# Kernel tuning notes

Hardware: AMD Instinct MI355X
Metric: run time of the kernel (lower is better)

Reference implementation:

```python
import jax, jax.numpy as jnp
import numpy as np

EPS = 1e-5
BS, NA, NC, NL, NPTS, ED, NG = 1, 900, 6, 4, 13, 256, 8
GD = ED // NG
IMG_W, IMG_H = 704.0, 256.0
FMAP_HW = [(64, 176), (32, 88), (16, 44), (8, 22)]


def _ln(x, g, b):
    m = x.mean(-1, keepdims=True)
    v = ((x - m) ** 2).mean(-1, keepdims=True)
    return (x - m) / jnp.sqrt(v + EPS) * g + b


def _grid_sample(img, grid):
    # img: [N,C,H,W]; grid: [N,P,Q,2] in [-1,1]; bilinear, zeros padding, align_corners=False
    N, C, H, W = img.shape
    gx = jnp.clip((grid[..., 0] + 1.0) * (W * 0.5) - 0.5, -1e4, 1e4)
    gy = jnp.clip((grid[..., 1] + 1.0) * (H * 0.5) - 0.5, -1e4, 1e4)
    x0 = jnp.floor(gx); y0 = jnp.floor(gy)
    wx1 = gx - x0; wy1 = gy - y0; wx0 = 1.0 - wx1; wy0 = 1.0 - wy1
    x0i = x0.astype(jnp.int32); y0i = y0.astype(jnp.int32)
    flat = img.reshape(N, C, H * W)

    def corner(xi, yi, wgt):
        valid = (xi >= 0) & (xi < W) & (yi >= 0) & (yi < H)
        idx = (jnp.clip(yi, 0, H - 1) * W + jnp.clip(xi, 0, W - 1))
        g = jax.vmap(lambda f, i: f[:, i])(flat, idx.reshape(N, -1))  # [N,C,P*Q]
        g = g.reshape(N, C, idx.shape[1], idx.shape[2])
        return g * (wgt * valid)[:, None]

    return (corner(x0i, y0i, wx0 * wy0) + corner(x0i + 1, y0i, wx1 * wy0)
            + corner(x0i, y0i + 1, wx0 * wy1) + corner(x0i + 1, y0i + 1, wx1 * wy1))


def setup_inputs() -> dict:
    key = jax.random.key(0)
    ks = jax.random.split(key, 20)
    d = {}
    d['instance_feature'] = jax.random.normal(ks[0], (BS, NA, ED), jnp.float32)
    xyz = jax.random.normal(ks[1], (BS, NA, 3), jnp.float32) * 1.5
    size = jax.random.normal(ks[2], (BS, NA, 3), jnp.float32) * 0.3
    theta = jax.random.uniform(ks[3], (BS, NA, 1), jnp.float32) * (2.0 * np.pi)
    vel = jax.random.normal(ks[4], (BS, NA, 3), jnp.float32) * 0.1
    d['anchor'] = jnp.concatenate([xyz, size, jnp.sin(theta), jnp.cos(theta), vel], -1)
    d['anchor_embed'] = jax.random.normal(ks[5], (BS, NA, ED), jnp.float32)
    for i, (h, w) in enumerate(FMAP_HW):
        d[f'fmap{i}'] = jax.random.normal(ks[6 + i], (BS, NC, ED, h, w), jnp.float32)
    base = jnp.array([[80., 0., 0., 352.], [0., 80., 0., 128.],
                      [0., 0., 0., 1.], [0., 0., 0., 1.]], jnp.float32)
    proj = jnp.tile(base, (BS, NC, 1, 1))
    proj = proj.at[:, :, :2, :].add(jax.random.normal(ks[10], (BS, NC, 2, 4), jnp.float32) * 2.0)
    d['projection_mat'] = proj
    d['image_wh'] = jnp.broadcast_to(jnp.array([IMG_W, IMG_H], jnp.float32), (BS, NC, 2))
    d['fix_scale'] = jnp.array([[0, 0, 0], [0.45, 0, 0], [-0.45, 0, 0], [0, 0.45, 0],
                                [0, -0.45, 0], [0, 0, 0.45], [0, 0, -0.45]], jnp.float32)

    def w(k, shape):
        return jax.random.normal(k, shape, jnp.float32) * 0.02

    d['lfc_w'] = w(ks[11], (ED, 6 * 3)); d['lfc_b'] = jnp.zeros((18,), jnp.float32)
    d['cam_w1'] = w(ks[12], (12, ED)); d['cam_b1'] = jnp.zeros((ED,), jnp.float32)
    d['cam_g1'] = jnp.ones((ED,), jnp.float32); d['cam_be1'] = jnp.zeros((ED,), jnp.float32)
    d['cam_w2'] = w(ks[13], (ED, ED)); d['cam_b2'] = jnp.zeros((ED,), jnp.float32)
    d['cam_g2'] = jnp.ones((ED,), jnp.float32); d['cam_be2'] = jnp.zeros((ED,), jnp.float32)
    d['wfc_w'] = w(ks[14], (ED, NG * NL * NPTS)); d['wfc_b'] = jnp.zeros((NG * NL * NPTS,), jnp.float32)
    d['op_w'] = w(ks[15], (ED, ED)); d['op_b'] = jnp.zeros((ED,), jnp.float32)
    return d


def reference(instance_feature, anchor, anchor_embed, fmap0, fmap1, fmap2, fmap3,
              projection_mat, image_wh, fix_scale, lfc_w, lfc_b,
              cam_w1, cam_b1, cam_g1, cam_be1, cam_w2, cam_b2, cam_g2, cam_be2,
              wfc_w, wfc_b, op_w, op_b):
    bs, na = instance_feature.shape[:2]
    # ---- keypoint generation ----
    size = jnp.exp(anchor[..., None, 3:6])                       # [bs,na,1,3]
    kp = fix_scale * size                                        # [bs,na,7,3]
    ls = jax.nn.sigmoid(instance_feature @ lfc_w + lfc_b).reshape(bs, na, -1, 3) - 0.5
    kp = jnp.concatenate([kp, ls * size], axis=-2)               # [bs,na,NPTS,3]
    sin, cos = anchor[..., 6:7], anchor[..., 7:8]                # [bs,na,1]
    kx, ky, kz = kp[..., 0], kp[..., 1], kp[..., 2]
    key_points = jnp.stack([cos * kx - sin * ky, sin * kx + cos * ky, kz], -1) \
                 + anchor[..., None, 0:3]                        # [bs,na,NPTS,3]
    # ---- per-cam/level/point group weights ----
    feat = instance_feature + anchor_embed
    cam_in = projection_mat[:, :, :3].reshape(bs, NC, 12)
    h = jax.nn.relu(cam_in @ cam_w1 + cam_b1); h = _ln(h, cam_g1, cam_be1)
    h = jax.nn.relu(h @ cam_w2 + cam_b2); cam_embed = _ln(h, cam_g2, cam_be2)
    f = feat[:, :, None] + cam_embed[:, None]                    # [bs,na,NC,ED]
    wts = (f @ wfc_w + wfc_b).reshape(bs, na, NC * NL * NPTS, NG)
    wts = jax.nn.softmax(wts, axis=-2).reshape(bs, na, NC, NL, NPTS, NG)
    # ---- multi-cam projection + bilinear sampling ----
    pts = jnp.concatenate([key_points, jnp.ones_like(key_points[..., :1])], -1)
    p2d = jnp.einsum('bcij,banj->bcani', projection_mat, pts)    # [bs,NC,na,NPTS,4]
    p2d = p2d[..., :2] / jnp.maximum(p2d[..., 2:3], 1e-5)
    p2d = p2d / image_wh[:, :, None, None]
    grid = (p2d * 2.0 - 1.0).reshape(bs * NC, na, NPTS, 2)
    feats = jnp.stack([_grid_sample(fm.reshape(bs * NC, ED, fm.shape[-2], fm.shape[-1]), grid)
                       for fm in (fmap0, fmap1, fmap2, fmap3)], axis=1)  # [bs*NC,NL,ED,na,NPTS]
    feats = feats.reshape(bs, NC, NL, ED, na, NPTS).transpose(0, 4, 1, 2, 5, 3)  # [bs,na,NC,NL,NPTS,ED]
    # ---- group-weighted fusion over cams & levels, then sum over points ----
    fg = feats.reshape(bs, na, NC, NL, NPTS, NG, GD)
    fused = jnp.einsum('bnclpg,bnclpgd->bnpgd', wts, fg).reshape(bs, na, NPTS, ED)
    fused = fused.sum(axis=2)                                    # [bs,na,ED]
    out = fused @ op_w + op_b
    return jnp.concatenate([out, instance_feature], axis=-1)     # [bs,na,2*ED]
```

## Files before the change

### kernel.cpp

```cpp
#include <hip/hip_runtime.h>
#include <stdint.h>

#define NA 900
#define NC 6
#define NL 4
#define NPTS 13
#define ED 256
#define NG 8
#define LNEPS 1e-5f
#define NSTAGE 718303
#define NSTAGE_BLOCKS 2806
#define NTRANS 5616
#define NSAMP 312

struct PIn { const void* p[24]; };

__device__ __forceinline__ float b2f(unsigned short u){
  union { uint32_t i; float f; } v; v.i = ((uint32_t)u)<<16; return v.f;
}
__device__ __forceinline__ unsigned short f2b(float f){
  union { float f; uint32_t i; } v; v.f = f;
  uint32_t r = v.i + 0x7FFFu + ((v.i>>16)&1u);
  return (unsigned short)(r>>16);
}
#define BLO(u) __uint_as_float((u)<<16)
#define BHI(u) __uint_as_float((u)&0xffff0000u)

__device__ __forceinline__ float ldx(const void* p, int i, bool bf){
  return bf ? b2f(((const unsigned short*)p)[i]) : ((const float*)p)[i];
}

__device__ __forceinline__ bool sniff_bf(const unsigned short* __restrict__ u16){
  int lane = threadIdx.x & 63;
  unsigned short u = u16[2*lane];
  int e = (u>>7)&0xFF;
  int sane = (e>=110 && e<=135) ? 1 : 0;
  #pragma unroll
  for (int m=32;m;m>>=1) sane += __shfl_xor(sane, m);
  return sane >= 48;
}

__device__ __forceinline__ void blockReduce2(float& a, float& b, float* lds){
  #pragma unroll
  for (int m=32;m;m>>=1){ a += __shfl_xor(a,m); b += __shfl_xor(b,m); }
  int w = threadIdx.x>>6;
  if ((threadIdx.x&63)==0){ lds[w]=a; lds[w+4]=b; }
  __syncthreads();
  a = lds[0]+lds[1]+lds[2]+lds[3];
  b = lds[4]+lds[5]+lds[6]+lds[7];
  __syncthreads();
}

__global__ __launch_bounds__(256) void k_prep(PIn in, float* __restrict__ stage,
                                              unsigned short* __restrict__ tf,
                                              float* __restrict__ Bc){
  const bool bf = sniff_bf((const unsigned short*)in.p[0]);
  const int tid = threadIdx.x;
  int b = blockIdx.x;

  __shared__ unsigned short T[64][68];
  __shared__ float h[ED];
  __shared__ float cE[ED];
  __shared__ float red8[8];
  __shared__ float part[4][64];

  if (b < NSTAGE_BLOCKS){
    const int cum[21] = {0,230400,240300,470700,470796,470808,470829,475437,475455,
                         478527,478783,479039,479295,544831,545087,545343,545599,
                         652095,652511,718047,718303};
    const int map[20] = {0,1,2,7,8,9,10,11,12,13,14,15,16,17,18,19,20,21,22,23};
    int idx = b*256 + tid;
    if (idx >= NSTAGE) return;
    int seg = 0, base = 0;
    #pragma unroll
    for (int s=1;s<20;s++) if (idx >= cum[s]){ seg = s; base = cum[s]; }
    const void* src = in.p[map[0]];
    #pragma unroll
    for (int s=1;s<20;s++) if (seg==s) src = in.p[map[s]];
    stage[idx] = ldx(src, idx - base, bf);
    return;
  }
  b -= NSTAGE_BLOCKS;
  if (b < NTRANS){
    const int xb[4]  = {176,44,11,3};
    const int HWs[4] = {11264,2816,704,176};
    const int TFO[4] = {0,17301504,21626880,22708224};
    int l, local;
    if      (b < 4224){ l=0; local=b;      }
    else if (b < 5280){ l=1; local=b-4224; }
    else if (b < 5544){ l=2; local=b-5280; }
    else              { l=3; local=b-5544; }
    int pt = local % xb[l]; int rest = local / xb[l];
    int ct = rest & 3; int c = rest >> 2;
    const int HW = HWs[l];
    const int px0 = pt*64;
    const void* src = in.p[3+l];
    #pragma unroll
    for (int p=0;p<2;p++){
      int lch = p*32 + (tid>>3);
      int gch = ct*64 + lch;
      int pxv = (tid&7)*8;
      size_t base = (size_t)(c*ED+gch)*HW + px0 + pxv;
      unsigned short v[8];
      if (px0 + pxv + 8 <= HW){
        if (bf){
          uint4 q = *reinterpret_cast<const uint4*>((const unsigned short*)src + base);
          v[0]=q.x&0xffff; v[1]=q.x>>16; v[2]=q.y&0xffff; v[3]=q.y>>16;
          v[4]=q.z&0xffff; v[5]=q.z>>16; v[6]=q.w&0xffff; v[7]=q.w>>16;
        } else {
          float4 f0 = *reinterpret_cast<const float4*>((const float*)src + base);
          float4 f1 = *reinterpret_cast<const float4*>((const float*)src + base + 4);
          v[0]=f2b(f0.x); v[1]=f2b(f0.y); v[2]=f2b(f0.z); v[3]=f2b(f0.w);
          v[4]=f2b(f1.x); v[5]=f2b(f1.y); v[6]=f2b(f1.z); v[7]=f2b(f1.w);
        }
      } else {
        #pragma unroll
        for (int i=0;i<8;i++){
          int px = px0+pxv+i;
          v[i] = (px<HW) ? (bf ? ((const unsigned short*)src)[base+i]
                               : f2b(((const float*)src)[base+i])) : (unsigned short)0;
        }
      }
      #pragma unroll
      for (int i=0;i<8;i++) T[pxv+i][lch] = v[i];
    }
    __syncthreads();
    unsigned short* dst = tf + TFO[l] + (size_t)c*HW*ED + ct*64;
    #pragma unroll
    for (int p=0;p<2;p++){
      int pxl = p*32 + (tid>>3);
      int px = px0 + pxl;
      if (px >= HW) continue;
      int ch8 = (tid&7)*8;
      ushort4 lo = *reinterpret_cast<ushort4*>(&T[pxl][ch8]);
      ushort4 hi = *reinterpret_cast<ushort4*>(&T[pxl][ch8+4]);
      union { ushort4 hh[2]; uint4 q; } u;
      u.hh[0]=lo; u.hh[1]=hi;
      *reinterpret_cast<uint4*>(dst + (size_t)px*ED + ch8) = u.q;
    }
    return;
  }
  b -= NTRANS;
  {
    const void* proj = in.p[7];
    const void* w1 = in.p[12]; const void* b1 = in.p[13];
    const void* g1 = in.p[14]; const void* be1 = in.p[15];
    const void* w2 = in.p[16]; const void* b2 = in.p[17];
    const void* g2 = in.p[18]; const void* be2 = in.p[19];
    const void* wfcw = in.p[20]; const void* wfcb = in.p[21];
    const int c = b/7, colt = b - (b/7)*7;
    float ci[12];
    #pragma unroll
    for (int i=0;i<12;i++) ci[i] = ldx(proj, c*16+i, bf);
    float acc = ldx(b1, tid, bf);
    #pragma unroll
    for (int k=0;k<12;k++) acc += ci[k]*ldx(w1, k*ED+tid, bf);
    float x = fmaxf(acc, 0.f);
    float s=x, q=x*x;
    blockReduce2(s,q,red8);
    float mean = s*(1.f/ED), var = q*(1.f/ED)-mean*mean;
    h[tid] = (x-mean)*rsqrtf(var+LNEPS)*ldx(g1,tid,bf) + ldx(be1,tid,bf);
    __syncthreads();
    acc = ldx(b2, tid, bf);
    #pragma unroll 8
    for (int k=0;k<ED;k++) acc += h[k]*ldx(w2, k*ED+tid, bf);
    x = fmaxf(acc,0.f);
    s=x; q=x*x;
    blockReduce2(s,q,red8);
    mean = s*(1.f/ED); var = q*(1.f/ED)-mean*mean;
    cE[tid] = (x-mean)*rsqrtf(var+LNEPS)*ldx(g2,tid,bf) + ldx(be2,tid,bf);
    __syncthreads();
    const int kc = tid>>6, colL = tid&63, col = colt*64+colL;
    float a = 0.f;
    if (col < 416){
      #pragma unroll 8
      for (int k=0;k<64;k++) a += cE[kc*64+k]*ldx(wfcw, (kc*64+k)*416+col, bf);
    }
    part[kc][colL] = a;
    __syncthreads();
    if (kc==0 && col<416)
      Bc[c*416+col] = part[0][colL]+part[1][colL]+part[2][colL]+part[3][colL] + ldx(wfcb,col,bf);
  }
}

__global__ __launch_bounds__(256) void k_anchor(
    const float* __restrict__ stage, const unsigned short* __restrict__ tf,
    const float* __restrict__ Bc, const void* __restrict__ rawinst,
    void* __restrict__ outv){
  const int n = blockIdx.x, tid = threadIdx.x;
  const bool bf = sniff_bf((const unsigned short*)rawinst);

  const float* s_inst = stage + 0;
  const float* s_anc  = stage + 230400;
  const float* s_ae   = stage + 240300;
  const float* s_proj = stage + 470700;
  const float* s_imwh = stage + 470796;
  const float* s_fixs = stage + 470808;
  const float* s_lw   = stage + 470829;
  const float* s_lb   = stage + 475437;
  const float* s_wfcw = stage + 545599;
  const float* s_opw  = stage + 652511;
  const float* s_opb  = stage + 718047;

  __shared__ float ifs[ED];
  __shared__ float fe[ED];
  __shared__ float lg[NC*416];
  __shared__ uint4 dsc[NSAMP*2];
  __shared__ float red[8][ED];
  __shared__ float fu[ED];
  __shared__ float kp[13][3];
  __shared__ float sc[8];
  __shared__ float lsv[18];

  {
    float iv = s_inst[n*ED+tid];
    ifs[tid] = iv;
    fe[tid]  = iv + s_ae[n*ED+tid];
    if (tid < 3)       sc[tid] = s_anc[n*11+tid];
    else if (tid == 3) sc[3]   = s_anc[n*11+6];
    else if (tid == 4) sc[4]   = s_anc[n*11+7];
    else if (tid < 8)  sc[tid] = __expf(s_anc[n*11+tid-2]);
  }
  __syncthreads();
  if (tid < 144){
    int d = tid>>3, j = tid&7;
    float a = 0.f;
    #pragma unroll 8
    for (int k=j*32;k<j*32+32;k++) a += ifs[k]*s_lw[k*18+d];
    a += __shfl_xor(a,1); a += __shfl_xor(a,2); a += __shfl_xor(a,4);
    if (j==0){
      a += s_lb[d];
      lsv[d] = 1.f/(1.f+__expf(-a)) - 0.5f;
    }
  }
  __syncthreads();
  if (tid < 13){
    float kx,ky,kz;
    if (tid < 7){
      kx = s_fixs[tid*3+0]*sc[5];
      ky = s_fixs[tid*3+1]*sc[6];
      kz = s_fixs[tid*3+2]*sc[7];
    } else {
      int j = tid-7;
      kx = lsv[j*3+0]*sc[5]; ky = lsv[j*3+1]*sc[6]; kz = lsv[j*3+2]*sc[7];
    }
    kp[tid][0] = sc[4]*kx - sc[3]*ky + sc[0];
    kp[tid][1] = sc[3]*kx + sc[4]*ky + sc[1];
    kp[tid][2] = kz + sc[2];
  }
  {
    int col2 = (tid < 160) ? tid+256 : 415;
    float a0 = 0.f, a1 = 0.f;
    #pragma unroll 4
    for (int k=0;k<ED;k++){
      float fv = fe[k];
      a0 += fv*s_wfcw[k*416+tid];
      a1 += fv*s_wfcw[k*416+col2];
    }
    #pragma unroll
    for (int c=0;c<NC;c++){
      lg[c*416+tid] = a0 + Bc[c*416+tid];
      if (tid < 160) lg[c*416+tid+256] = a1 + Bc[c*416+tid+256];
    }
  }
  __syncthreads();
  #pragma unroll
  for (int pass=0;pass<2;pass++){
    int s = tid + pass*256;
    if (s < NSAMP){
      int c = s/52, rr = s - c*52;
      int l = rr/13, p = rr - l*13;
      float m[12];
      #pragma unroll
      for (int i=0;i<12;i++) m[i] = s_proj[c*16+i];
      float X=kp[p][0], Y=kp[p][1], Z=kp[p][2];
      float x = m[0]*X + m[1]*Y + m[2]*Z  + m[3];
      float y = m[4]*X + m[5]*Y + m[6]*Z  + m[7];
      float z = m[8]*X + m[9]*Y + m[10]*Z + m[11];
      float d = fmaxf(z, 1e-5f);
      float px = x/(d*s_imwh[c*2+0]), py = y/(d*s_imwh[c*2+1]);
      const int W = 176>>l, H = 64>>l;
      const int TFO[4] = {0,17301504,21626880,22708224};
      float gx = fminf(fmaxf(px*(float)W - 0.5f, -10000.f), 10000.f);
      float gy = fminf(fmaxf(py*(float)H - 0.5f, -10000.f), 10000.f);
      float xf = floorf(gx), yf = floorf(gy);
      int x0 = (int)xf, y0 = (int)yf;
      float wx1 = gx-xf, wy1 = gy-yf;
      float wx0 = 1.f-wx1, wy0 = 1.f-wy1;
      bool vx0 = (x0>=0)&&(x0<W),   vx1 = (x0+1>=0)&&(x0+1<W);
      bool vy0 = (y0>=0)&&(y0<H),   vy1 = (y0+1>=0)&&(y0+1<H);
      float w00 = (vx0&&vy0) ? wx0*wy0 : 0.f;
      float w10 = (vx1&&vy0) ? wx1*wy0 : 0.f;
      float w01 = (vx0&&vy1) ? wx0*wy1 : 0.f;
      float w11 = (vx1&&vy1) ? wx1*wy1 : 0.f;
      int cx0 = min(max(x0,0),W-1), cx1 = min(max(x0+1,0),W-1);
      int cy0 = min(max(y0,0),H-1), cy1 = min(max(y0+1,0),H-1);
      uint32_t cam = (uint32_t)TFO[l] + (uint32_t)(c*H*W)*ED;
      uint4 bi, wv;
      bi.x = cam + (uint32_t)(cy0*W+cx0)*ED;
      bi.y = cam + (uint32_t)(cy0*W+cx1)*ED;
      bi.z = cam + (uint32_t)(cy1*W+cx0)*ED;
      bi.w = cam + (uint32_t)(cy1*W+cx1)*ED;
      wv.x = __float_as_uint(w00); wv.y = __float_as_uint(w10);
      wv.z = __float_as_uint(w01); wv.w = __float_as_uint(w11);
      dsc[s*2]   = bi;
      dsc[s*2+1] = wv;
    }
  }
  {
    const int g = tid>>5, j = tid&31;
    float v[10]; float m = -1e30f;
    #pragma unroll
    for (int i=0;i<10;i++){
      int e = j + 32*i;
      float val = -1e30f;
      if (e < NSAMP){
        int c = e/52, rr = e - c*52;
        val = lg[c*416 + rr*8 + g];
        m = fmaxf(m, val);
      }
      v[i] = val;
    }
    #pragma unroll
    for (int mk=16;mk;mk>>=1) m = fmaxf(m, __shfl_xor(m, mk, 32));
    float sum = 0.f;
    #pragma unroll
    for (int i=0;i<10;i++){
      if (j + 32*i < NSAMP){ float ex = __expf(v[i]-m); v[i] = ex; sum += ex; }
    }
    #pragma unroll
    for (int mk=16;mk;mk>>=1) sum += __shfl_xor(sum, mk, 32);
    float inv = 1.f/sum;
    #pragma unroll
    for (int i=0;i<10;i++){
      int e = j + 32*i;
      if (e < NSAMP){
        int c = e/52, rr = e - c*52;
        lg[c*416 + rr*8 + g] = v[i]*inv;
      }
    }
  }
  __syncthreads();
  {
    const int strm = tid>>5, lane32 = tid&31;
    const int ch8 = lane32*8, gg = lane32>>2;
    float acc[8] = {0,0,0,0,0,0,0,0};
    for (int it=0; it<39; it++){
      int s = it*8 + strm;
      uint4 bi = dsc[s*2];
      uint4 wf = dsc[s*2+1];
      float w00 = __uint_as_float(wf.x), w10 = __uint_as_float(wf.y);
      float w01 = __uint_as_float(wf.z), w11 = __uint_as_float(wf.w);
      if (w00+w10+w01+w11 == 0.f) continue;
      int c = s/52, rr = s - c*52;
      float wg = lg[c*416 + rr*8 + gg];
      uint4 q00 = *reinterpret_cast<const uint4*>(tf + bi.x + ch8);
      uint4 q10 = *reinterpret_cast<const uint4*>(tf + bi.y + ch8);
      uint4 q01 = *reinterpret_cast<const uint4*>(tf + bi.z + ch8);
      uint4 q11 = *reinterpret_cast<const uint4*>(tf + bi.w + ch8);
      acc[0] += wg*(w00*BLO(q00.x)+w10*BLO(q10.x)+w01*BLO(q01.x)+w11*BLO(q11.x));
      acc[1] += wg*(w00*BHI(q00.x)+w10*BHI(q10.x)+w01*BHI(q01.x)+w11*BHI(q11.x));
      acc[2] += wg*(w00*BLO(q00.y)+w10*BLO(q10.y)+w01*BLO(q01.y)+w11*BLO(q11.y));
      acc[3] += wg*(w00*BHI(q00.y)+w10*BHI(q10.y)+w01*BHI(q01.y)+w11*BHI(q11.y));
      acc[4] += wg*(w00*BLO(q00.z)+w10*BLO(q10.z)+w01*BLO(q01.z)+w11*BLO(q11.z));
      acc[5] += wg*(w00*BHI(q00.z)+w10*BHI(q10.z)+w01*BHI(q01.z)+w11*BHI(q11.z));
      acc[6] += wg*(w00*BLO(q00.w)+w10*BLO(q10.w)+w01*BLO(q01.w)+w11*BLO(q11.w));
      acc[7] += wg*(w00*BHI(q00.w)+w10*BHI(q10.w)+w01*BHI(q01.w)+w11*BHI(q11.w));
    }
    *reinterpret_cast<float4*>(&red[strm][ch8])   = make_float4(acc[0],acc[1],acc[2],acc[3]);
    *reinterpret_cast<float4*>(&red[strm][ch8+4]) = make_float4(acc[4],acc[5],acc[6],acc[7]);
  }
  __syncthreads();
  {
    float r = 0.f;
    #pragma unroll
    for (int i=0;i<8;i++) r += red[i][tid];
    fu[tid] = r;
  }
  __syncthreads();
  {
    float acc = s_opb[tid];
    #pragma unroll 4
    for (int k=0;k<ED;k++) acc += fu[k]*s_opw[k*ED+tid];
    float pv = ifs[tid];
    if (bf){
      unsigned short* outh = (unsigned short*)outv;
      outh[n*512+tid]     = f2b(acc);
      outh[n*512+256+tid] = f2b(pv);
    } else {
      float* outf = (float*)outv;
      outf[n*512+tid]     = acc;
      outf[n*512+256+tid] = pv;
    }
  }
}

extern "C" void kernel_launch(void* const* d_in, const int* in_sizes, int n_in,
                              void* d_out, int out_size, void* d_ws, size_t ws_size,
                              hipStream_t stream){
  char* ws = (char*)d_ws;
  size_t off = 0;
  auto alloc = [&](size_t bytes)->char*{
    char* p = ws + off; off += (bytes + 63) & ~size_t(63); return p;
  };
  unsigned short* tf = (unsigned short*)alloc((size_t)22978560*2);
  float* stage  = (float*)alloc((size_t)NSTAGE*4);
  float* Bc     = (float*)alloc((size_t)NC*416*4);

  PIn in;
  for (int i=0;i<24;i++) in.p[i] = d_in[i];

  k_prep<<<NSTAGE_BLOCKS + NTRANS + 42, 256, 0, stream>>>(in, stage, tf, Bc);
  k_anchor<<<NA, 256, 0, stream>>>(stage, tf, Bc, d_in[0], d_out);
}
```

Before: 257.1 us.

## Store weights as bf16, compact valid samples, and unroll gather loop by two

The prep kernel gains a block range that converts the fc and output-projection weight matrices to bf16 copies, so each anchor block reads half the weight bytes in its two dense matvecs. The anchor kernel now compacts only samples with nonzero bilinear weight into a shared list via an atomic counter, skipping invalid samples without a per-iteration branch. The gather loop processes two samples per iteration to expose more outstanding loads. The cost is extra rounding of weights to bf16 even when the inputs are fp32, and a nondeterministic sample order that changes floating-point summation order.

```diff
diff --git a/kernel.cpp b/kernel.cpp
--- a/kernel.cpp
+++ b/kernel.cpp
@@ -11,6 +11,7 @@
 #define NSTAGE 718303
 #define NSTAGE_BLOCKS 2806
 #define NTRANS 5616
+#define NCOPY 672
 #define NSAMP 312
 
 struct PIn { const void* p[24]; };
@@ -53,6 +54,8 @@
 
 __global__ __launch_bounds__(256) void k_prep(PIn in, float* __restrict__ stage,
                                               unsigned short* __restrict__ tf,
+                                              unsigned short* __restrict__ wfcw_h,
+                                              unsigned short* __restrict__ opw_h,
                                               float* __restrict__ Bc){
   const bool bf = sniff_bf((const unsigned short*)in.p[0]);
   const int tid = threadIdx.x;
@@ -141,6 +144,19 @@
     return;
   }
   b -= NTRANS;
+  if (b < NCOPY){
+    int idx = b*256 + tid;
+    if (idx < 106496){
+      wfcw_h[idx] = bf ? ((const unsigned short*)in.p[20])[idx]
+                       : f2b(((const float*)in.p[20])[idx]);
+    } else {
+      int j = idx - 106496;
+      opw_h[j] = bf ? ((const unsigned short*)in.p[22])[j]
+                    : f2b(((const float*)in.p[22])[j]);
+    }
+    return;
+  }
+  b -= NCOPY;
   {
     const void* proj = in.p[7];
     const void* w1 = in.p[12]; const void* b1 = in.p[13];
@@ -185,6 +201,7 @@
 
 __global__ __launch_bounds__(256) void k_anchor(
     const float* __restrict__ stage, const unsigned short* __restrict__ tf,
+    const unsigned short* __restrict__ wfcw_h, const unsigned short* __restrict__ opw_h,
     const float* __restrict__ Bc, const void* __restrict__ rawinst,
     void* __restrict__ outv){
   const int n = blockIdx.x, tid = threadIdx.x;
@@ -198,21 +215,23 @@
   const float* s_fixs = stage + 470808;
   const float* s_lw   = stage + 470829;
   const float* s_lb   = stage + 475437;
-  const float* s_wfcw = stage + 545599;
-  const float* s_opw  = stage + 652511;
   const float* s_opb  = stage + 718047;
 
   __shared__ float ifs[ED];
   __shared__ float fe[ED];
   __shared__ float lg[NC*416];
-  __shared__ uint4 dsc[NSAMP*2];
-  __shared__ float red[8][ED];
+  __shared__ uint4 cbi[NSAMP];
+  __shared__ uint4 cwf[NSAMP];
+  __shared__ unsigned short coff[NSAMP];
+  __shared__ float red[8][ED+4];
   __shared__ float fu[ED];
   __shared__ float kp[13][3];
   __shared__ float sc[8];
   __shared__ float lsv[18];
-
-  {
+  __shared__ int scnt;
+
+  {
+    if (tid==0) scnt = 0;
     float iv = s_inst[n*ED+tid];
     ifs[tid] = iv;
     fe[tid]  = iv + s_ae[n*ED+tid];
@@ -254,8 +273,8 @@
     #pragma unroll 4
     for (int k=0;k<ED;k++){
       float fv = fe[k];
-      a0 += fv*s_wfcw[k*416+tid];
-      a1 += fv*s_wfcw[k*416+col2];
+      a0 += fv*b2f(wfcw_h[k*416+tid]);
+      a1 += fv*b2f(wfcw_h[k*416+col2]);
     }
     #pragma unroll
     for (int c=0;c<NC;c++){
@@ -293,18 +312,22 @@
       float w10 = (vx1&&vy0) ? wx1*wy0 : 0.f;
       float w01 = (vx0&&vy1) ? wx0*wy1 : 0.f;
       float w11 = (vx1&&vy1) ? wx1*wy1 : 0.f;
-      int cx0 = min(max(x0,0),W-1), cx1 = min(max(x0+1,0),W-1);
-      int cy0 = min(max(y0,0),H-1), cy1 = min(max(y0+1,0),H-1);
-      uint32_t cam = (uint32_t)TFO[l] + (uint32_t)(c*H*W)*ED;
-      uint4 bi, wv;
-      bi.x = cam + (uint32_t)(cy0*W+cx0)*ED;
-      bi.y = cam + (uint32_t)(cy0*W+cx1)*ED;
-      bi.z = cam + (uint32_t)(cy1*W+cx0)*ED;
-      bi.w = cam + (uint32_t)(cy1*W+cx1)*ED;
-      wv.x = __float_as_uint(w00); wv.y = __float_as_uint(w10);
-      wv.z = __float_as_uint(w01); wv.w = __float_as_uint(w11);
-      dsc[s*2]   = bi;
-      dsc[s*2+1] = wv;
+      if (w00+w10+w01+w11 != 0.f){
+        int cx0 = min(max(x0,0),W-1), cx1 = min(max(x0+1,0),W-1);
+        int cy0 = min(max(y0,0),H-1), cy1 = min(max(y0+1,0),H-1);
+        uint32_t cam = (uint32_t)TFO[l] + (uint32_t)(c*H*W)*ED;
+        uint4 bi, wv;
+        bi.x = cam + (uint32_t)(cy0*W+cx0)*ED;
+        bi.y = cam + (uint32_t)(cy0*W+cx1)*ED;
+        bi.z = cam + (uint32_t)(cy1*W+cx0)*ED;
+        bi.w = cam + (uint32_t)(cy1*W+cx1)*ED;
+        wv.x = __float_as_uint(w00); wv.y = __float_as_uint(w10);
+        wv.z = __float_as_uint(w01); wv.w = __float_as_uint(w11);
+        int slot = atomicAdd(&scnt, 1);
+        cbi[slot] = bi;
+        cwf[slot] = wv;
+        coff[slot] = (unsigned short)(c*416 + rr*8);
+      }
     }
   }
   {
@@ -342,30 +365,61 @@
   }
   __syncthreads();
   {
+    const int m = scnt;
     const int strm = tid>>5, lane32 = tid&31;
     const int ch8 = lane32*8, gg = lane32>>2;
     float acc[8] = {0,0,0,0,0,0,0,0};
-    for (int it=0; it<39; it++){
-      int s = it*8 + strm;
-      uint4 bi = dsc[s*2];
-      uint4 wf = dsc[s*2+1];
-      float w00 = __uint_as_float(wf.x), w10 = __uint_as_float(wf.y);
-      float w01 = __uint_as_float(wf.z), w11 = __uint_as_float(wf.w);
-      if (w00+w10+w01+w11 == 0.f) continue;
-      int c = s/52, rr = s - c*52;
-      float wg = lg[c*416 + rr*8 + gg];
+    int i = strm;
+    for (; i + 8 < m; i += 16){
+      uint4 biA = cbi[i],   wfA = cwf[i];
+      uint4 biB = cbi[i+8], wfB = cwf[i+8];
+      float wgA = lg[coff[i]+gg],  wgB = lg[coff[i+8]+gg];
+      uint4 a00 = *reinterpret_cast<const uint4*>(tf + biA.x + ch8);
+      uint4 a10 = *reinterpret_cast<const uint4*>(tf + biA.y + ch8);
+      uint4 a01 = *reinterpret_cast<const uint4*>(tf + biA.z + ch8);
+      uint4 a11 = *reinterpret_cast<const uint4*>(tf + biA.w + ch8);
+      uint4 b00 = *reinterpret_cast<const uint4*>(tf + biB.x + ch8);
+      uint4 b10 = *reinterpret_cast<const uint4*>(tf + biB.y + ch8);
+      uint4 b01 = *reinterpret_cast<const uint4*>(tf + biB.z + ch8);
+      uint4 b11 = *reinterpret_cast<const uint4*>(tf + biB.w + ch8);
+      float pA00 = wgA*__uint_as_float(wfA.x), pA10 = wgA*__uint_as_float(wfA.y);
+      float pA01 = wgA*__uint_as_float(wfA.z), pA11 = wgA*__uint_as_float(wfA.w);
+      float pB00 = wgB*__uint_as_float(wfB.x), pB10 = wgB*__uint_as_float(wfB.y);
+      float pB01 = wgB*__uint_as_float(wfB.z), pB11 = wgB*__uint_as_float(wfB.w);
+      acc[0] += pA00*BLO(a00.x)+pA10*BLO(a10.x)+pA01*BLO(a01.x)+pA11*BLO(a11.x)
+              + pB00*BLO(b00.x)+pB10*BLO(b10.x)+pB01*BLO(b01.x)+pB11*BLO(b11.x);
+      acc[1] += pA00*BHI(a00.x)+pA10*BHI(a10.x)+pA01*BHI(a01.x)+pA11*BHI(a11.x)
+              + pB00*BHI(b00.x)+pB10*BHI(b10.x)+pB01*BHI(b01.x)+pB11*BHI(b11.x);
+      acc[2] += pA00*BLO(a00.y)+pA10*BLO(a10.y)+pA01*BLO(a01.y)+pA11*BLO(a11.y)
+              + pB00*BLO(b00.y)+pB10*BLO(b10.y)+pB01*BLO(b01.y)+pB11*BLO(b11.y);
+      acc[3] += pA00*BHI(a00.y)+pA10*BHI(a10.y)+pA01*BHI(a01.y)+pA11*BHI(a11.y)
+              + pB00*BHI(b00.y)+pB10*BHI(b10.y)+pB01*BHI(b01.y)+pB11*BHI(b11.y);
+      acc[4] += pA00*BLO(a00.z)+pA10*BLO(a10.z)+pA01*BLO(a01.z)+pA11*BLO(a11.z)
+              + pB00*BLO(b00.z)+pB10*BLO(b10.z)+pB01*BLO(b01.z)+pB11*BLO(b11.z);
+      acc[5] += pA00*BHI(a00.z)+pA10*BHI(a10.z)+pA01*BHI(a01.z)+pA11*BHI(a11.z)
+              + pB00*BHI(b00.z)+pB10*BHI(b10.z)+pB01*BHI(b01.z)+pB11*BHI(b11.z);
+      acc[6] += pA00*BLO(a00.w)+pA10*BLO(a10.w)+pA01*BLO(a01.w)+pA11*BLO(a11.w)
+              + pB00*BLO(b00.w)+pB10*BLO(b10.w)+pB01*BLO(b01.w)+pB11*BLO(b11.w);
+      acc[7] += pA00*BHI(a00.w)+pA10*BHI(a10.w)+pA01*BHI(a01.w)+pA11*BHI(a11.w)
+              + pB00*BHI(b00.w)+pB10*BHI(b10.w)+pB01*BHI(b01.w)+pB11*BHI(b11.w);
+    }
+    for (; i < m; i += 8){
+      uint4 bi = cbi[i], wf = cwf[i];
+      float wg = lg[coff[i]+gg];
       uint4 q00 = *reinterpret_cast<const uint4*>(tf + bi.x + ch8);
       uint4 q10 = *reinterpret_cast<const uint4*>(tf + bi.y + ch8);
       uint4 q01 = *reinterpret_cast<const uint4*>(tf + bi.z + ch8);
       uint4 q11 = *reinterpret_cast<const uint4*>(tf + bi.w + ch8);
-      acc[0] += wg*(w00*BLO(q00.x)+w10*BLO(q10.x)+w01*BLO(q01.x)+w11*BLO(q11.x));
-      acc[1] += wg*(w00*BHI(q00.x)+w10*BHI(q10.x)+w01*BHI(q01.x)+w11*BHI(q11.x));
-      acc[2] += wg*(w00*BLO(q00.y)+w10*BLO(q10.y)+w01*BLO(q01.y)+w11*BLO(q11.y));
-      acc[3] += wg*(w00*BHI(q00.y)+w10*BHI(q10.y)+w01*BHI(q01.y)+w11*BHI(q11.y));
-      acc[4] += wg*(w00*BLO(q00.z)+w10*BLO(q10.z)+w01*BLO(q01.z)+w11*BLO(q11.z));
-      acc[5] += wg*(w00*BHI(q00.z)+w10*BHI(q10.z)+w01*BHI(q01.z)+w11*BHI(q11.z));
-      acc[6] += wg*(w00*BLO(q00.w)+w10*BLO(q10.w)+w01*BLO(q01.w)+w11*BLO(q11.w));
-      acc[7] += wg*(w00*BHI(q00.w)+w10*BHI(q10.w)+w01*BHI(q01.w)+w11*BHI(q11.w));
+      float p00 = wg*__uint_as_float(wf.x), p10 = wg*__uint_as_float(wf.y);
+      float p01 = wg*__uint_as_float(wf.z), p11 = wg*__uint_as_float(wf.w);
+      acc[0] += p00*BLO(q00.x)+p10*BLO(q10.x)+p01*BLO(q01.x)+p11*BLO(q11.x);
+      acc[1] += p00*BHI(q00.x)+p10*BHI(q10.x)+p01*BHI(q01.x)+p11*BHI(q11.x);
+      acc[2] += p00*BLO(q00.y)+p10*BLO(q10.y)+p01*BLO(q01.y)+p11*BLO(q11.y);
+      acc[3] += p00*BHI(q00.y)+p10*BHI(q10.y)+p01*BHI(q01.y)+p11*BHI(q11.y);
+      acc[4] += p00*BLO(q00.z)+p10*BLO(q10.z)+p01*BLO(q01.z)+p11*BLO(q11.z);
+      acc[5] += p00*BHI(q00.z)+p10*BHI(q10.z)+p01*BHI(q01.z)+p11*BHI(q11.z);
+      acc[6] += p00*BLO(q00.w)+p10*BLO(q10.w)+p01*BLO(q01.w)+p11*BLO(q11.w);
+      acc[7] += p00*BHI(q00.w)+p10*BHI(q10.w)+p01*BHI(q01.w)+p11*BHI(q11.w);
     }
     *reinterpret_cast<float4*>(&red[strm][ch8])   = make_float4(acc[0],acc[1],acc[2],acc[3]);
     *reinterpret_cast<float4*>(&red[strm][ch8+4]) = make_float4(acc[4],acc[5],acc[6],acc[7]);
@@ -381,7 +435,7 @@
   {
     float acc = s_opb[tid];
     #pragma unroll 4
-    for (int k=0;k<ED;k++) acc += fu[k]*s_opw[k*ED+tid];
+    for (int k=0;k<ED;k++) acc += fu[k]*b2f(opw_h[k*ED+tid]);
     float pv = ifs[tid];
     if (bf){
       unsigned short* outh = (unsigned short*)outv;
@@ -405,11 +459,13 @@
   };
   unsigned short* tf = (unsigned short*)alloc((size_t)22978560*2);
   float* stage  = (float*)alloc((size_t)NSTAGE*4);
+  unsigned short* wfcw_h = (unsigned short*)alloc((size_t)106496*2);
+  unsigned short* opw_h  = (unsigned short*)alloc((size_t)65536*2);
   float* Bc     = (float*)alloc((size_t)NC*416*4);
 
   PIn in;
   for (int i=0;i<24;i++) in.p[i] = d_in[i];
 
-  k_prep<<<NSTAGE_BLOCKS + NTRANS + 42, 256, 0, stream>>>(in, stage, tf, Bc);
-  k_anchor<<<NA, 256, 0, stream>>>(stage, tf, Bc, d_in[0], d_out);
-}
+  k_prep<<<NSTAGE_BLOCKS + NTRANS + NCOPY + 42, 256, 0, stream>>>(in, stage, tf, wfcw_h, opw_h, Bc);
+  k_anchor<<<NA, 256, 0, stream>>>(stage, tf, wfcw_h, opw_h, Bc, d_in[0], d_out);
+}
```

Result: no change. 253.1 us (-1.6%).
